# Performance work log

Hardware: AMD Instinct MI355X
Metric: run time of the kernel (lower is better)

The kernel has to match this reference:

```python
import jax, jax.numpy as jnp
import numpy as np

NQ = 8
NL = 6
DIM = 2 ** NQ
C64 = jnp.complex64
I2 = jnp.eye(2, dtype=C64)
PX = jnp.array([[0., 1.], [1., 0.]], dtype=C64)
PY = jnp.array([[0., -1j], [1j, 0.]], dtype=C64)
PZ = jnp.array([[1., 0.], [0., -1.]], dtype=C64)
# sign of Pauli-Z eigenvalue for each computational basis state, wires 0..3 (wire 0 = MSB)
_idx = np.arange(DIM)
_SIGNS = jnp.asarray(np.stack([1.0 - 2.0 * ((_idx >> (NQ - 1 - w)) & 1) for w in range(4)]).astype(np.float32))  # (4, 256)

def _rot(t, P):
    # exp(-i t/2 P) = cos(t/2) I - i sin(t/2) P
    th = t.astype(jnp.float32) / 2
    return jnp.cos(th) * I2 - 1j * jnp.sin(th) * P

def _apply1(st, U, w):
    # apply 2x2 unitary U on wire w; st: (B, 2,2,...,2)
    s = jnp.moveaxis(st, w + 1, -1)
    return jnp.moveaxis(s @ U.T, -1, w + 1)

def _cnot(st, c, t):
    # flip target axis where control bit == 1
    s = jnp.moveaxis(st, (c + 1, t + 1), (1, 2))
    s = jnp.concatenate([s[:, :1], s[:, 1:, ::-1]], axis=1)
    return jnp.moveaxis(s, (1, 2), (c + 1, t + 1))

def _quantum(x, weights):
    B = x.shape[0]
    # AmplitudeEmbedding with normalize=True
    psi = (x / jnp.linalg.norm(x, axis=1, keepdims=True)).astype(C64)
    st = psi.reshape((B,) + (2,) * NQ)
    for l in range(NL):
        lw = weights[l]
        for q in range(NQ):
            st = _apply1(st, _rot(lw[3 * q], PX), q)
            st = _apply1(st, _rot(lw[3 * q + 1], PY), q)
            st = _apply1(st, _rot(lw[3 * q + 2], PZ), q)
        for i in range(NQ - 1):
            st = _cnot(st, i, i + 1)
        st = _cnot(st, NQ - 1, 0)
        for i in range(0, NQ, 2):
            if i + 2 < NQ:
                st = _cnot(st, i, i + 2)
    probs = jnp.abs(st.reshape(B, DIM)) ** 2
    return probs @ _SIGNS.T  # (B, 4) Z expectations on wires 0..3

def _bn(h, g, b):
    # BatchNorm1d, training mode (batch statistics, biased variance)
    m = h.mean(0)
    v = h.var(0)
    return g * (h - m) * jax.lax.rsqrt(v + 1e-5) + b

def _forward(x, q_weights, aW, ab, fW1, fb1, fW2, fb2, cW1, cb1, g1, be1, cW2, cb2, g2, be2, cW3, cb3, cW4, cb4):
    q = _quantum(x, q_weights)                     # (B, 4)
    qf = q @ aW.T + ab                             # quantum_adapter
    cf = jnp.tanh(jax.nn.relu(x @ fW1.T + fb1) @ fW2.T + fb2)  # feature_processor
    h = qf + cf
    h = jax.nn.relu(_bn(h @ cW1.T + cb1, g1, be1))
    h = jax.nn.relu(_bn(h @ cW2.T + cb2, g2, be2))
    h = jax.nn.relu(h @ cW3.T + cb3)
    return jax.nn.sigmoid(h @ cW4.T + cb4)         # (B, 1)

def setup_inputs():
    key = jax.random.key(0)
    ks = jax.random.split(key, 21)
    f32 = jnp.float32
    r = lambda k, shp, s: jax.random.normal(k, shp, dtype=f32) * s
    B = 8192
    return {
        'x': r(ks[0], (B, 256), 1.0),
        'q_weights': r(ks[1], (NL, NQ * 3), 1.0),
        'aW': r(ks[2], (4, 4), 0.5), 'ab': r(ks[3], (4,), 0.1),
        'fW1': r(ks[4], (64, 256), 0.0625), 'fb1': r(ks[5], (64,), 0.05),
        'fW2': r(ks[6], (4, 64), 0.125), 'fb2': r(ks[7], (4,), 0.05),
        'cW1': r(ks[8], (32, 4), 0.5), 'cb1': r(ks[9], (32,), 0.05),
        'g1': 1.0 + r(ks[10], (32,), 0.05), 'be1': r(ks[11], (32,), 0.05),
        'cW2': r(ks[12], (16, 32), 0.18), 'cb2': r(ks[13], (16,), 0.05),
        'g2': 1.0 + r(ks[14], (16,), 0.05), 'be2': r(ks[15], (16,), 0.05),
        'cW3': r(ks[16], (8, 16), 0.25), 'cb3': r(ks[17], (8,), 0.05),
        'cW4': r(ks[18], (1, 8), 0.35), 'cb4': r(ks[19], (1,), 0.05),
    }

def reference(x, q_weights, aW, ab, fW1, fb1, fW2, fb2, cW1, cb1, g1, be1, cW2, cb2, g2, be2, cW3, cb3, cW4, cb4):
    return _forward(x, q_weights, aW, ab, fW1, fb1, fW2, fb2, cW1, cb1, g1, be1, cW2, cb2, g2, be2, cW3, cb3, cW4, cb4)
```

## Files before the change

### kernel.cpp

```cpp
#include <hip/hip_runtime.h>
#include <math.h>

#define INV_B (1.0f / 8192.0f)

typedef float  v2f  __attribute__((ext_vector_type(2)));
typedef _Float16 half8 __attribute__((ext_vector_type(8)));
typedef float  f32x4 __attribute__((ext_vector_type(4)));
typedef unsigned u32x4 __attribute__((ext_vector_type(4)));

struct QTables {
    int xm[6][8];
    int rm[6][8];
    int meas[4];
};
constexpr QTables make_tables() {
    QTables T{};
    int Mrow[8] = {}, Ncol[8] = {};
    for (int b = 0; b < 8; ++b) { Mrow[b] = 1 << b; Ncol[b] = 1 << b; }
    constexpr int bc[11] = {7,6,5,4,3,2,1,0,7,5,3};
    constexpr int bt[11] = {6,5,4,3,2,1,0,7,5,3,1};
    for (int l = 0; l < 6; ++l) {
        for (int w = 0; w < 8; ++w) { T.xm[l][w] = Ncol[7 - w]; T.rm[l][w] = Mrow[7 - w]; }
        for (int k = 0; k < 11; ++k) { Mrow[bt[k]] ^= Mrow[bc[k]]; Ncol[bc[k]] ^= Ncol[bt[k]]; }
    }
    for (int w = 0; w < 4; ++w) T.meas[w] = Mrow[7 - w];
    return T;
}
constexpr QTables TB = make_tables();

template<int ML>
static __device__ __forceinline__ float lanex(float v) {
    if constexpr (ML == 0) { return v; }
    else if constexpr (ML == 1) { return __int_as_float(__builtin_amdgcn_update_dpp(0, __float_as_int(v), 0xB1, 0xF, 0xF, true)); }
    else if constexpr (ML == 2) { return __int_as_float(__builtin_amdgcn_update_dpp(0, __float_as_int(v), 0x4E, 0xF, 0xF, true)); }
    else if constexpr (ML == 3) { return __int_as_float(__builtin_amdgcn_update_dpp(0, __float_as_int(v), 0x1B, 0xF, 0xF, true)); }
    else if constexpr (ML < 32) { return __int_as_float(__builtin_amdgcn_ds_swizzle(__float_as_int(v), 0x1F | (ML << 10))); }
    else { return __shfl_xor(v, ML, 64); }
}

static __device__ __forceinline__ float tanh_fast(float v) {
    const float c = fminf(fmaxf(v, -10.f), 10.f);
    const float e = __expf(2.f * c);
    return (e - 1.f) / (e + 1.f);
}

static __device__ __forceinline__ void coh_store_h(_Float16* p, _Float16 v) {
    __hip_atomic_store((short*)p, __builtin_bit_cast(short, v),
                       __ATOMIC_RELAXED, __HIP_MEMORY_SCOPE_AGENT);
}
static __device__ __forceinline__ void coh_store_f(float* p, float v) {
    __hip_atomic_store(p, v, __ATOMIC_RELAXED, __HIP_MEMORY_SCOPE_AGENT);
}
static __device__ __forceinline__ float coh_load_f(const float* p) {
    return __hip_atomic_load(p, __ATOMIC_RELAXED, __HIP_MEMORY_SCOPE_AGENT);
}

template<int XM, int RM>
static __device__ __forceinline__ void gate(v2f (&z)[4], const int lane,
                                            const float u00r, const float u00i,
                                            const float u01r, const float u01i) {
    constexpr int ML = XM >> 2, MR = XM & 3;
    constexpr int RL = RM >> 2, RR = RM & 3;
    const int pl = __popc(lane & RL) & 1;
    const float csi0 = pl ? -u00i : u00i;
    const float cpr0 = pl ? -u01r : u01r;
    const float csi1 = -csi0, cpr1 = -cpr0;
    v2f p[4];
    #pragma unroll
    for (int r = 0; r < 4; ++r) {
        p[r].x = lanex<ML>(z[r ^ MR].x);
        p[r].y = lanex<ML>(z[r ^ MR].y);
    }
    #pragma unroll
    for (int r = 0; r < 4; ++r) {
        const int pb = __builtin_popcount(r & RR) & 1;
        const float csi = pb ? csi1 : csi0;
        const float cpr = pb ? cpr1 : cpr0;
        const v2f zs = { -z[r].y, z[r].x };
        const v2f ps = { -p[r].y, p[r].x };
        z[r] = ((u00r * z[r] + csi * zs) + cpr * p[r]) + u01i * ps;
    }
}

static __device__ __forceinline__ void gbar(unsigned* arr, unsigned* rel) {
    __syncthreads();
    if (blockIdx.x == 0) {
        if (threadIdx.x != 0) {
            while (!__hip_atomic_load(&arr[threadIdx.x], __ATOMIC_RELAXED,
                                      __HIP_MEMORY_SCOPE_AGENT))
                __builtin_amdgcn_s_sleep(2);
        }
        __syncthreads();
        if (threadIdx.x < 16)
            __hip_atomic_store(&rel[threadIdx.x * 16], 1u, __ATOMIC_RELAXED,
                               __HIP_MEMORY_SCOPE_AGENT);
        __syncthreads();
    } else {
        if (threadIdx.x == 0) {
            __hip_atomic_store(&arr[blockIdx.x], 1u, __ATOMIC_RELAXED,
                               __HIP_MEMORY_SCOPE_AGENT);
            unsigned* myrel = rel + (blockIdx.x & 15) * 16;
            while (!__hip_atomic_load(myrel, __ATOMIC_RELAXED, __HIP_MEMORY_SCOPE_AGENT))
                __builtin_amdgcn_s_sleep(2);
        }
        __syncthreads();
    }
}

#define XS 264

#define ISS(B, pr, pi) asm volatile( \
    "global_load_dwordx4 %0, %16, off sc1\n\t" \
    "global_load_dwordx4 %1, %16, off offset:64 sc1\n\t" \
    "global_load_dwordx4 %2, %16, off offset:128 sc1\n\t" \
    "global_load_dwordx4 %3, %16, off offset:192 sc1\n\t" \
    "global_load_dwordx4 %4, %16, off offset:256 sc1\n\t" \
    "global_load_dwordx4 %5, %16, off offset:320 sc1\n\t" \
    "global_load_dwordx4 %6, %16, off offset:384 sc1\n\t" \
    "global_load_dwordx4 %7, %16, off offset:448 sc1\n\t" \
    "global_load_dwordx4 %8, %17, off sc1\n\t" \
    "global_load_dwordx4 %9, %17, off offset:64 sc1\n\t" \
    "global_load_dwordx4 %10, %17, off offset:128 sc1\n\t" \
    "global_load_dwordx4 %11, %17, off offset:192 sc1\n\t" \
    "global_load_dwordx4 %12, %17, off offset:256 sc1\n\t" \
    "global_load_dwordx4 %13, %17, off offset:320 sc1\n\t" \
    "global_load_dwordx4 %14, %17, off offset:384 sc1\n\t" \
    "global_load_dwordx4 %15, %17, off offset:448 sc1" \
    : "=&v"(B##0), "=&v"(B##1), "=&v"(B##2), "=&v"(B##3), \
      "=&v"(B##4), "=&v"(B##5), "=&v"(B##6), "=&v"(B##7), \
      "=&v"(B##8), "=&v"(B##9), "=&v"(B##10), "=&v"(B##11), \
      "=&v"(B##12), "=&v"(B##13), "=&v"(B##14), "=&v"(B##15) \
    : "v"(pr), "v"(pi) : "memory")

#define WAIT16 do { asm volatile("s_waitcnt vmcnt(16)" ::: "memory"); \
                    __builtin_amdgcn_sched_barrier(0); } while (0)
#define WAIT0  do { asm volatile("s_waitcnt vmcnt(0)" ::: "memory"); \
                    __builtin_amdgcn_sched_barrier(0); } while (0)

#define MF(A, Bv, C) __builtin_amdgcn_mfma_f32_16x16x32_f16((A), \
                        __builtin_bit_cast(half8, (Bv)), (C), 0, 0, 0)

#define CMP(B, CC) { \
    f32x4 cr0 = {0.f,0.f,0.f,0.f}, ci0 = {0.f,0.f,0.f,0.f}; \
    f32x4 cr1 = {0.f,0.f,0.f,0.f}, ci1 = {0.f,0.f,0.f,0.f}; \
    cr0 = MF(af[0], B##0, cr0);  ci0 = MF(af[0], B##8,  ci0); \
    cr1 = MF(af[4], B##4, cr1);  ci1 = MF(af[4], B##12, ci1); \
    cr0 = MF(af[1], B##1, cr0);  ci0 = MF(af[1], B##9,  ci0); \
    cr1 = MF(af[5], B##5, cr1);  ci1 = MF(af[5], B##13, ci1); \
    cr0 = MF(af[2], B##2, cr0);  ci0 = MF(af[2], B##10, ci0); \
    cr1 = MF(af[6], B##6, cr1);  ci1 = MF(af[6], B##14, ci1); \
    cr0 = MF(af[3], B##3, cr0);  ci0 = MF(af[3], B##11, ci0); \
    cr1 = MF(af[7], B##7, cr1);  ci1 = MF(af[7], B##15, ci1); \
    const int c_ = whalf * 8 + (CC); \
    float sgn_[4]; \
    _Pragma("unroll") \
    for (int mw = 0; mw < 4; ++mw) { \
        const int scw = __builtin_popcount((c_ * 16) & TB.meas[mw]) & 1; \
        sgn_[mw] = (slm[mw] ^ scw) ? -1.f : 1.f; \
    } \
    _Pragma("unroll") \
    for (int r = 0; r < 4; ++r) { \
        const float re = cr0[r] + cr1[r], im = ci0[r] + ci1[r]; \
        const float p = re * re + im * im; \
        sS[r] += p; \
        _Pragma("unroll") \
        for (int mw = 0; mw < 4; ++mw) sq[mw][r] = fmaf(sgn_[mw], p, sq[mw][r]); \
    } \
}

__global__ __launch_bounds__(256, 1) void k_fused(
        const float* __restrict__ x, const float* __restrict__ qw,
        const float* __restrict__ fW1, const float* __restrict__ fb1,
        const float* __restrict__ fW2, const float* __restrict__ fb2,
        const float* __restrict__ aW, const float* __restrict__ ab,
        const float* __restrict__ cW1, const float* __restrict__ cb1,
        const float* __restrict__ g1, const float* __restrict__ be1,
        const float* __restrict__ cW2, const float* __restrict__ cb2,
        const float* __restrict__ g2, const float* __restrict__ be2,
        const float* __restrict__ cW3, const float* __restrict__ cb3,
        const float* __restrict__ cW4, const float* __restrict__ cb4,
        _Float16* __restrict__ Wt, float* __restrict__ acc1,
        float* __restrict__ acc2, unsigned* __restrict__ bar,
        float* __restrict__ out)
{
    const int t = threadIdx.x, b = blockIdx.x;
    const int lane = t & 63, w = t >> 6;
    const int R0 = b * 32;

    __shared__ _Float16 xa[32 * XS];
    __shared__ float4 Us[48];
    __shared__ float cfb[32][4];
    __shared__ float hb[32][4];
    __shared__ float z2b[32][16];
    __shared__ float pS[32];
    __shared__ float pQ[4][32];
    __shared__ float sA[20];
    __shared__ float m1s[32], is1[32];
    __shared__ float sB[32];
    __shared__ float m2s[16], is2[16];

    #pragma unroll
    for (int i = 0; i < 8; ++i) {
        const int idx = i * 256 + t;
        const int row = idx >> 6, c4 = idx & 63;
        const float4 xv = ((const float4*)(x + (long)(R0 + row) * 256))[c4];
        _Float16* d = &xa[row * XS + c4 * 4];
        d[0] = (_Float16)xv.x; d[1] = (_Float16)xv.y;
        d[2] = (_Float16)xv.z; d[3] = (_Float16)xv.w;
    }
    if (t < 48) {
        const int l = t >> 3, q = t & 7;
        const float* a = qw + l * 24 + q * 3;
        const float h1 = 0.5f * a[0], h2 = 0.5f * a[1], h3 = 0.5f * a[2];
        const float c1 = cosf(h1), s1 = sinf(h1);
        const float c2 = cosf(h2), s2 = sinf(h2);
        const float c3 = cosf(h3), s3 = sinf(h3);
        const float m00r =  c1 * c2, m00i =  s1 * s2;
        const float m01r = -c1 * s2, m01i = -s1 * c2;
        float4 u;
        u.x = m00r * c3 + m00i * s3;  u.y = m00i * c3 - m00r * s3;
        u.z = m01r * c3 + m01i * s3;  u.w = m01i * c3 - m01r * s3;
        Us[t] = u;
    }
    if (t >= 192 && t < 224) {
        const int r = t - 192;
        pS[r] = 0.f;
        pQ[0][r] = 0.f; pQ[1][r] = 0.f; pQ[2][r] = 0.f; pQ[3][r] = 0.f;
    }
    if (b < 32 && w == 3) {
        const int l = t - 192;
        if (l < 20) coh_store_f(&acc1[b * 20 + l], 0.f);
        if (l < 32) coh_store_f(&acc2[b * 32 + l], 0.f);
    }
    __syncthreads();

    if (w == 0) {
        const int k = b;
        v2f z[4];
        #pragma unroll
        for (int r = 0; r < 4; ++r) {
            z[r].x = (4 * lane + r == k) ? 1.f : 0.f;
            z[r].y = 0.f;
        }
#define GATE(L, W) { const float4 u = Us[(L) * 8 + (W)]; \
                     gate<TB.xm[L][W], TB.rm[L][W]>(z, lane, u.x, u.y, u.z, u.w); }
#define LAYER(L) GATE(L,0) GATE(L,1) GATE(L,2) GATE(L,3) GATE(L,4) GATE(L,5) GATE(L,6) GATE(L,7)
        LAYER(0) LAYER(1) LAYER(2) LAYER(3) LAYER(4) LAYER(5)
#undef LAYER
#undef GATE
        #pragma unroll
        for (int r = 0; r < 4; ++r) {
            const int i = 4 * lane + r;
            coh_store_h(&Wt[(long)i * 256 + k],         (_Float16)z[r].x);
            coh_store_h(&Wt[(long)(256 + i) * 256 + k], (_Float16)z[r].y);
        }
    } else if (w <= 2) {
        const int g = lane >> 4, col = lane & 15;
        const int mt = w - 1;
        half8 bf[8];
        #pragma unroll
        for (int kb = 0; kb < 8; ++kb)
            bf[kb] = *(const half8*)&xa[(mt * 16 + col) * XS + kb * 32 + g * 8];
        float accc[4] = {0.f, 0.f, 0.f, 0.f};
        #pragma unroll
        for (int jc = 0; jc < 4; ++jc) {
            f32x4 cv = {0.f, 0.f, 0.f, 0.f};
            #pragma unroll
            for (int kb = 0; kb < 8; ++kb) {
                const float* ap = fW1 + (long)(jc * 16 + col) * 256 + kb * 32 + g * 8;
                const float4 a0 = *(const float4*)ap;
                const float4 a1v = *(const float4*)(ap + 4);
                half8 af;
                af[0] = (_Float16)a0.x;  af[1] = (_Float16)a0.y;
                af[2] = (_Float16)a0.z;  af[3] = (_Float16)a0.w;
                af[4] = (_Float16)a1v.x; af[5] = (_Float16)a1v.y;
                af[6] = (_Float16)a1v.z; af[7] = (_Float16)a1v.w;
                cv = __builtin_amdgcn_mfma_f32_16x16x32_f16(af, bf[kb], cv, 0, 0, 0);
            }
            #pragma unroll
            for (int r = 0; r < 4; ++r) {
                const int j = jc * 16 + g * 4 + r;
                const float z = fmaxf(cv[r] + fb1[j], 0.f);
                #pragma unroll
                for (int c = 0; c < 4; ++c) accc[c] += z * fW2[c * 64 + j];
            }
        }
        #pragma unroll
        for (int c = 0; c < 4; ++c) {
            accc[c] += __shfl_xor(accc[c], 16, 64);
            accc[c] += __shfl_xor(accc[c], 32, 64);
        }
        if (g == 0) {
            cfb[mt * 16 + col][0] = tanh_fast(accc[0] + fb2[0]);
            cfb[mt * 16 + col][1] = tanh_fast(accc[1] + fb2[1]);
            cfb[mt * 16 + col][2] = tanh_fast(accc[2] + fb2[2]);
            cfb[mt * 16 + col][3] = tanh_fast(accc[3] + fb2[3]);
        }
    }

    gbar(bar, bar + 768);

    {
        const int col = lane & 15, quad = lane >> 4;
        const int wrow = w & 1;
        const int whalf = w >> 1;
        half8 af[8];
        #pragma unroll
        for (int kb = 0; kb < 8; ++kb)
            af[kb] = *(const half8*)&xa[(wrow * 16 + col) * XS + kb * 32 + quad * 8];

        int slm[4];
        #pragma unroll
        for (int mw = 0; mw < 4; ++mw) slm[mw] = __popc(col & TB.meas[mw]) & 1;

        float sS[4] = {0.f, 0.f, 0.f, 0.f};
        float sq[4][4] = {{0.f}};
        const _Float16* pre = Wt + (long)col * 256 + quad * 8 + (long)(whalf * 8) * 4096;
        const _Float16* pim = pre + 65536;

        u32x4 BA0, BA1, BA2, BA3, BA4, BA5, BA6, BA7;
        u32x4 BA8, BA9, BA10, BA11, BA12, BA13, BA14, BA15;
        u32x4 BB0, BB1, BB2, BB3, BB4, BB5, BB6, BB7;
        u32x4 BB8, BB9, BB10, BB11, BB12, BB13, BB14, BB15;

        ISS(BA, pre,            pim);
        ISS(BB, pre + 1 * 4096, pim + 1 * 4096);
        WAIT16; CMP(BA, 0);
        ISS(BA, pre + 2 * 4096, pim + 2 * 4096);
        WAIT16; CMP(BB, 1);
        ISS(BB, pre + 3 * 4096, pim + 3 * 4096);
        WAIT16; CMP(BA, 2);
        ISS(BA, pre + 4 * 4096, pim + 4 * 4096);
        WAIT16; CMP(BB, 3);
        ISS(BB, pre + 5 * 4096, pim + 5 * 4096);
        WAIT16; CMP(BA, 4);
        ISS(BA, pre + 6 * 4096, pim + 6 * 4096);
        WAIT16; CMP(BB, 5);
        ISS(BB, pre + 7 * 4096, pim + 7 * 4096);
        WAIT16; CMP(BA, 6);
        WAIT0;  CMP(BB, 7);

        #pragma unroll
        for (int r = 0; r < 4; ++r) {
            sS[r] += lanex<1>(sS[r]); sS[r] += lanex<2>(sS[r]);
            sS[r] += lanex<4>(sS[r]); sS[r] += lanex<8>(sS[r]);
            #pragma unroll
            for (int mw = 0; mw < 4; ++mw) {
                sq[mw][r] += lanex<1>(sq[mw][r]); sq[mw][r] += lanex<2>(sq[mw][r]);
                sq[mw][r] += lanex<4>(sq[mw][r]); sq[mw][r] += lanex<8>(sq[mw][r]);
            }
        }

        if (col == 0) {
            #pragma unroll
            for (int r = 0; r < 4; ++r) {
                const int mloc = wrow * 16 + quad * 4 + r;
                atomicAdd(&pS[mloc], sS[r]);
                #pragma unroll
                for (int mw = 0; mw < 4; ++mw) atomicAdd(&pQ[mw][mloc], sq[mw][r]);
            }
        }
    }
    __syncthreads();
    if (t < 32) {
        const float inv = 1.0f / pS[t];
        float qe[4];
        #pragma unroll
        for (int mw = 0; mw < 4; ++mw) qe[mw] = pQ[mw][t] * inv;
        #pragma unroll
        for (int kk = 0; kk < 4; ++kk) {
            float s = ab[kk] + cfb[t][kk];
            #pragma unroll
            for (int j = 0; j < 4; ++j) s += aW[kk * 4 + j] * qe[j];
            hb[t][kk] = s;
        }
    }
    __syncthreads();
    if (t < 20) {
        const int j = (t - 4) >> 2, kk = (t - 4) & 3;
        float v = 0.f;
        for (int rr = 0; rr < 32; ++rr)
            v += (t < 4) ? hb[rr][t] : hb[rr][j] * hb[rr][kk];
        atomicAdd(acc1 + (b & 31) * 20 + t, v);
    }

    gbar(bar + 256, bar + 1024);

    if (t < 20) {
        float s = 0.f;
        for (int sl = 0; sl < 32; ++sl) s += coh_load_f(&acc1[sl * 20 + t]);
        sA[t] = s;
    }
    __syncthreads();
    if (t < 32) {
        float mu[4], wv[4];
        #pragma unroll
        for (int k = 0; k < 4; ++k) mu[k] = sA[k] * INV_B;
        float m = cb1[t];
        #pragma unroll
        for (int k = 0; k < 4; ++k) { wv[k] = cW1[t * 4 + k]; m += wv[k] * mu[k]; }
        float var = 0.f;
        #pragma unroll
        for (int a2 = 0; a2 < 4; ++a2)
            #pragma unroll
            for (int b2 = 0; b2 < 4; ++b2)
                var += wv[a2] * wv[b2] * (sA[4 + a2 * 4 + b2] * INV_B - mu[a2] * mu[b2]);
        m1s[t] = m;
        is1[t] = 1.0f / sqrtf(var + 1e-5f);
    }
    __syncthreads();

    {
        const int row = t & 31, grp = t >> 5;
        const float h0 = hb[row][0], h1 = hb[row][1], h2 = hb[row][2], h3 = hb[row][3];
        float a1[32];
        #pragma unroll
        for (int j = 0; j < 32; ++j) {
            float zz = cb1[j] + cW1[j * 4 + 0] * h0 + cW1[j * 4 + 1] * h1
                              + cW1[j * 4 + 2] * h2 + cW1[j * 4 + 3] * h3;
            a1[j] = fmaxf((zz - m1s[j]) * is1[j] * g1[j] + be1[j], 0.f);
        }
        #pragma unroll
        for (int d = 0; d < 2; ++d) {
            const int kk = grp * 2 + d;
            float s = cb2[kk];
            #pragma unroll
            for (int j = 0; j < 32; ++j) s += cW2[kk * 32 + j] * a1[j];
            z2b[row][kk] = s;
        }
    }
    __syncthreads();
    if (t < 32) {
        const int colz = t & 15, mode = t >> 4;
        float s = 0.f;
        for (int rr = 0; rr < 32; ++rr) {
            const float v = z2b[rr][colz];
            s += mode ? v * v : v;
        }
        atomicAdd(acc2 + (b & 31) * 32 + mode * 16 + colz, s);
    }

    gbar(bar + 512, bar + 1280);

    if (t < 32) {
        float s = 0.f;
        for (int sl = 0; sl < 32; ++sl) s += coh_load_f(&acc2[sl * 32 + t]);
        sB[t] = s;
    }
    __syncthreads();
    if (t < 16) {
        const float m = sB[t] * INV_B;
        const float var = sB[16 + t] * INV_B - m * m;
        m2s[t] = m;
        is2[t] = 1.0f / sqrtf(var + 1e-5f);
    }
    __syncthreads();
    if (t < 32) {
        float a2[16];
        #pragma unroll
        for (int k = 0; k < 16; ++k)
            a2[k] = fmaxf((z2b[t][k] - m2s[k]) * is2[k] * g2[k] + be2[k], 0.f);
        float z3[8];
        #pragma unroll
        for (int j = 0; j < 8; ++j) {
            float s = cb3[j];
            #pragma unroll
            for (int k = 0; k < 16; ++k) s += cW3[j * 16 + k] * a2[k];
            z3[j] = fmaxf(s, 0.f);
        }
        float y = cb4[0];
        #pragma unroll
        for (int j = 0; j < 8; ++j) y += cW4[j] * z3[j];
        out[R0 + t] = 1.0f / (1.0f + expf(-y));
    }
}

extern "C" void kernel_launch(void* const* d_in, const int* in_sizes, int n_in,
                              void* d_out, int out_size, void* d_ws, size_t ws_size,
                              hipStream_t stream) {
    (void)in_sizes; (void)n_in; (void)out_size; (void)ws_size;
    const float* x   = (const float*)d_in[0];
    const float* qw  = (const float*)d_in[1];
    const float* aW  = (const float*)d_in[2];
    const float* ab  = (const float*)d_in[3];
    const float* fW1 = (const float*)d_in[4];
    const float* fb1 = (const float*)d_in[5];
    const float* fW2 = (const float*)d_in[6];
    const float* fb2 = (const float*)d_in[7];
    const float* cW1 = (const float*)d_in[8];
    const float* cb1 = (const float*)d_in[9];
    const float* g1  = (const float*)d_in[10];
    const float* be1 = (const float*)d_in[11];
    const float* cW2 = (const float*)d_in[12];
    const float* cb2 = (const float*)d_in[13];
    const float* g2  = (const float*)d_in[14];
    const float* be2 = (const float*)d_in[15];
    const float* cW3 = (const float*)d_in[16];
    const float* cb3 = (const float*)d_in[17];
    const float* cW4 = (const float*)d_in[18];
    const float* cb4 = (const float*)d_in[19];

    float* ws    = (float*)d_ws;
    float* acc1  = ws;
    float* acc2  = ws + 1024;
    unsigned* bar = (unsigned*)(ws + 2048);
    _Float16* Wt = (_Float16*)(ws + 215040);
    float* outp  = (float*)d_out;

    hipMemsetAsync(bar, 0, 6144, stream);
    k_fused<<<256, 256, 0, stream>>>(x, qw, fW1, fb1, fW2, fb2, aW, ab,
                                     cW1, cb1, g1, be1, cW2, cb2, g2, be2,
                                     cW3, cb3, cW4, cb4, Wt, acc1, acc2, bar, outp);
}
```

Measured before the change: 132.5 us.

## Have each wave cover both row tiles to halve global W loads

```diff
diff --git a/kernel.cpp b/kernel.cpp
--- a/kernel.cpp
+++ b/kernel.cpp
@@ -140,18 +140,18 @@
 #define MF(A, Bv, C) __builtin_amdgcn_mfma_f32_16x16x32_f16((A), \
                         __builtin_bit_cast(half8, (Bv)), (C), 0, 0, 0)
 
-#define CMP(B, CC) { \
+#define CMP(B, CC, WR) { \
     f32x4 cr0 = {0.f,0.f,0.f,0.f}, ci0 = {0.f,0.f,0.f,0.f}; \
     f32x4 cr1 = {0.f,0.f,0.f,0.f}, ci1 = {0.f,0.f,0.f,0.f}; \
-    cr0 = MF(af[0], B##0, cr0);  ci0 = MF(af[0], B##8,  ci0); \
-    cr1 = MF(af[4], B##4, cr1);  ci1 = MF(af[4], B##12, ci1); \
-    cr0 = MF(af[1], B##1, cr0);  ci0 = MF(af[1], B##9,  ci0); \
-    cr1 = MF(af[5], B##5, cr1);  ci1 = MF(af[5], B##13, ci1); \
-    cr0 = MF(af[2], B##2, cr0);  ci0 = MF(af[2], B##10, ci0); \
-    cr1 = MF(af[6], B##6, cr1);  ci1 = MF(af[6], B##14, ci1); \
-    cr0 = MF(af[3], B##3, cr0);  ci0 = MF(af[3], B##11, ci0); \
-    cr1 = MF(af[7], B##7, cr1);  ci1 = MF(af[7], B##15, ci1); \
-    const int c_ = whalf * 8 + (CC); \
+    cr0 = MF(af[(WR)*8+0], B##0, cr0);  ci0 = MF(af[(WR)*8+0], B##8,  ci0); \
+    cr1 = MF(af[(WR)*8+4], B##4, cr1);  ci1 = MF(af[(WR)*8+4], B##12, ci1); \
+    cr0 = MF(af[(WR)*8+1], B##1, cr0);  ci0 = MF(af[(WR)*8+1], B##9,  ci0); \
+    cr1 = MF(af[(WR)*8+5], B##5, cr1);  ci1 = MF(af[(WR)*8+5], B##13, ci1); \
+    cr0 = MF(af[(WR)*8+2], B##2, cr0);  ci0 = MF(af[(WR)*8+2], B##10, ci0); \
+    cr1 = MF(af[(WR)*8+6], B##6, cr1);  ci1 = MF(af[(WR)*8+6], B##14, ci1); \
+    cr0 = MF(af[(WR)*8+3], B##3, cr0);  ci0 = MF(af[(WR)*8+3], B##11, ci0); \
+    cr1 = MF(af[(WR)*8+7], B##7, cr1);  ci1 = MF(af[(WR)*8+7], B##15, ci1); \
+    const int c_ = cbase + (CC); \
     float sgn_[4]; \
     _Pragma("unroll") \
     for (int mw = 0; mw < 4; ++mw) { \
@@ -162,9 +162,9 @@
     for (int r = 0; r < 4; ++r) { \
         const float re = cr0[r] + cr1[r], im = ci0[r] + ci1[r]; \
         const float p = re * re + im * im; \
-        sS[r] += p; \
+        sS[WR][r] += p; \
         _Pragma("unroll") \
-        for (int mw = 0; mw < 4; ++mw) sq[mw][r] = fmaf(sgn_[mw], p, sq[mw][r]); \
+        for (int mw = 0; mw < 4; ++mw) sq[WR][mw][r] = fmaf(sgn_[mw], p, sq[WR][mw][r]); \
     } \
 }
 
@@ -302,20 +302,21 @@
 
     {
         const int col = lane & 15, quad = lane >> 4;
-        const int wrow = w & 1;
-        const int whalf = w >> 1;
-        half8 af[8];
-        #pragma unroll
-        for (int kb = 0; kb < 8; ++kb)
-            af[kb] = *(const half8*)&xa[(wrow * 16 + col) * XS + kb * 32 + quad * 8];
+        const int cbase = w * 4;
+        half8 af[16];
+        #pragma unroll
+        for (int wr = 0; wr < 2; ++wr)
+            #pragma unroll
+            for (int kb = 0; kb < 8; ++kb)
+                af[wr * 8 + kb] = *(const half8*)&xa[(wr * 16 + col) * XS + kb * 32 + quad * 8];
 
         int slm[4];
         #pragma unroll
         for (int mw = 0; mw < 4; ++mw) slm[mw] = __popc(col & TB.meas[mw]) & 1;
 
-        float sS[4] = {0.f, 0.f, 0.f, 0.f};
-        float sq[4][4] = {{0.f}};
-        const _Float16* pre = Wt + (long)col * 256 + quad * 8 + (long)(whalf * 8) * 4096;
+        float sS[2][4] = {{0.f}};
+        float sq[2][4][4] = {{{0.f}}};
+        const _Float16* pre = Wt + (long)col * 256 + quad * 8 + (long)cbase * 4096;
         const _Float16* pim = pre + 65536;
 
         u32x4 BA0, BA1, BA2, BA3, BA4, BA5, BA6, BA7;
@@ -325,40 +326,38 @@
 
         ISS(BA, pre,            pim);
         ISS(BB, pre + 1 * 4096, pim + 1 * 4096);
-        WAIT16; CMP(BA, 0);
+        WAIT16; CMP(BA, 0, 0); CMP(BA, 0, 1);
         ISS(BA, pre + 2 * 4096, pim + 2 * 4096);
-        WAIT16; CMP(BB, 1);
+        WAIT16; CMP(BB, 1, 0); CMP(BB, 1, 1);
         ISS(BB, pre + 3 * 4096, pim + 3 * 4096);
-        WAIT16; CMP(BA, 2);
-        ISS(BA, pre + 4 * 4096, pim + 4 * 4096);
-        WAIT16; CMP(BB, 3);
-        ISS(BB, pre + 5 * 4096, pim + 5 * 4096);
-        WAIT16; CMP(BA, 4);
-        ISS(BA, pre + 6 * 4096, pim + 6 * 4096);
-        WAIT16; CMP(BB, 5);
-        ISS(BB, pre + 7 * 4096, pim + 7 * 4096);
-        WAIT16; CMP(BA, 6);
-        WAIT0;  CMP(BB, 7);
-
-        #pragma unroll
-        for (int r = 0; r < 4; ++r) {
-            sS[r] += lanex<1>(sS[r]); sS[r] += lanex<2>(sS[r]);
-            sS[r] += lanex<4>(sS[r]); sS[r] += lanex<8>(sS[r]);
-            #pragma unroll
-            for (int mw = 0; mw < 4; ++mw) {
-                sq[mw][r] += lanex<1>(sq[mw][r]); sq[mw][r] += lanex<2>(sq[mw][r]);
-                sq[mw][r] += lanex<4>(sq[mw][r]); sq[mw][r] += lanex<8>(sq[mw][r]);
+        WAIT16; CMP(BA, 2, 0); CMP(BA, 2, 1);
+        WAIT0;  CMP(BB, 3, 0); CMP(BB, 3, 1);
+
+        #pragma unroll
+        for (int wr = 0; wr < 2; ++wr)
+            #pragma unroll
+            for (int r = 0; r < 4; ++r) {
+                sS[wr][r] += lanex<1>(sS[wr][r]); sS[wr][r] += lanex<2>(sS[wr][r]);
+                sS[wr][r] += lanex<4>(sS[wr][r]); sS[wr][r] += lanex<8>(sS[wr][r]);
+                #pragma unroll
+                for (int mw = 0; mw < 4; ++mw) {
+                    sq[wr][mw][r] += lanex<1>(sq[wr][mw][r]);
+                    sq[wr][mw][r] += lanex<2>(sq[wr][mw][r]);
+                    sq[wr][mw][r] += lanex<4>(sq[wr][mw][r]);
+                    sq[wr][mw][r] += lanex<8>(sq[wr][mw][r]);
+                }
             }
-        }
 
         if (col == 0) {
             #pragma unroll
-            for (int r = 0; r < 4; ++r) {
-                const int mloc = wrow * 16 + quad * 4 + r;
-                atomicAdd(&pS[mloc], sS[r]);
+            for (int wr = 0; wr < 2; ++wr)
                 #pragma unroll
-                for (int mw = 0; mw < 4; ++mw) atomicAdd(&pQ[mw][mloc], sq[mw][r]);
-            }
+                for (int r = 0; r < 4; ++r) {
+                    const int mloc = wr * 16 + quad * 4 + r;
+                    atomicAdd(&pS[mloc], sS[wr][r]);
+                    #pragma unroll
+                    for (int mw = 0; mw < 4; ++mw) atomicAdd(&pQ[mw][mloc], sq[wr][mw][r]);
+                }
         }
     }
     __syncthreads();
```

Measured after the change: 127.3 us, median of 2. 1.04x faster.
